# Kernel optimization log

Measured on AMD Instinct MI355X. Metric: run time of the kernel, lower is better.

The kernel has to match this reference:

```python
import jax, jax.numpy as jnp
import numpy as np

N_NODES = 50000
N_EDGES = 1600000
NFEAT = 256
NHID = 32
HEADS = 8
NCLASS = 2
NEG_SLOPE = 0.2  # DGL GATConv default


def gat_layer(x, src, dst, W, al, ar, b, num_nodes):
    """DGL-style GATConv layer.
    x: [N, in], W: [in, H*F], al/ar: [H, F], b: [H*F].
    Returns [N, H*F].
    """
    H, F = al.shape
    feat = (x @ W).reshape(num_nodes, H, F)          # [N, H, F]
    el = jnp.einsum('nhf,hf->nh', feat, al)          # [N, H]
    er = jnp.einsum('nhf,hf->nh', feat, ar)          # [N, H]
    e = jax.nn.leaky_relu(el[src] + er[dst], NEG_SLOPE)  # [E, H]
    # segment softmax over incoming edges of each dst node
    m = jax.ops.segment_max(e, dst, num_segments=num_nodes)  # [N, H]
    m = jnp.where(jnp.isfinite(m), m, 0.0)
    m = jax.lax.stop_gradient(m)
    ee = jnp.exp(e - m[dst])                          # [E, H]
    denom = jax.ops.segment_sum(ee, dst, num_segments=num_nodes)  # [N, H]
    alpha = ee / jnp.maximum(denom[dst], 1e-16)       # [E, H]
    # weighted scatter-aggregation of source features
    msg = feat[src] * alpha[:, :, None]               # [E, H, F]
    out = jax.ops.segment_sum(msg, dst, num_segments=num_nodes)  # [N, H, F]
    return out.reshape(num_nodes, H * F) + b


def setup_inputs() -> dict:
    key = jax.random.key(0)
    ks = jax.random.split(key, 10)
    x = jax.random.normal(ks[0], (N_NODES, NFEAT), dtype=jnp.float32)
    edge_src = jax.random.randint(ks[1], (N_EDGES,), 0, N_NODES, dtype=jnp.int32)
    edge_dst = jax.random.randint(ks[2], (N_EDGES,), 0, N_NODES, dtype=jnp.int32)
    s1 = 1.0 / np.sqrt(NFEAT)
    W1 = jax.random.normal(ks[3], (NFEAT, HEADS * NHID), dtype=jnp.float32) * s1
    al1 = jax.random.normal(ks[4], (HEADS, NHID), dtype=jnp.float32) * 0.1
    ar1 = jax.random.normal(ks[5], (HEADS, NHID), dtype=jnp.float32) * 0.1
    b1 = jnp.zeros((HEADS * NHID,), dtype=jnp.float32)
    s2 = 1.0 / np.sqrt(HEADS * NHID)
    W2 = jax.random.normal(ks[6], (HEADS * NHID, NCLASS), dtype=jnp.float32) * s2
    al2 = jax.random.normal(ks[7], (1, NCLASS), dtype=jnp.float32) * 0.1
    ar2 = jax.random.normal(ks[8], (1, NCLASS), dtype=jnp.float32) * 0.1
    b2 = jnp.zeros((NCLASS,), dtype=jnp.float32)
    return {"x": x, "edge_src": edge_src, "edge_dst": edge_dst,
            "W1": W1, "al1": al1, "ar1": ar1, "b1": b1,
            "W2": W2, "al2": al2, "ar2": ar2, "b2": b2}


def reference(x, edge_src, edge_dst, W1, al1, ar1, b1, W2, al2, ar2, b2):
    h = gat_layer(x, edge_src, edge_dst, W1, al1, ar1, b1, N_NODES)  # [N, 8*nhid]
    h = jax.nn.elu(h)
    h = gat_layer(h, edge_src, edge_dst, W2, al2, ar2, b2, N_NODES)  # [N, nclass]
    return jax.nn.log_softmax(h, axis=1)
```

## Files before the change

kernel.cpp:

```cpp
#include <hip/hip_runtime.h>
#include <hip/hip_fp8.h>


#define NN 50000
#define NE 1600000
#define NBK 196
#define NPB 1024
#define PCH 1563
#define CAP 16384

typedef __attribute__((ext_vector_type(8))) short short8;
typedef __attribute__((ext_vector_type(4))) float f32x4;
typedef __attribute__((ext_vector_type(2))) float f32x2;

__device__ inline unsigned short f2bf(float f) {
  unsigned int u = __float_as_uint(f);
  unsigned int r = (u + 0x7fffu + ((u >> 16) & 1u)) >> 16;
  return (unsigned short)r;
}
__device__ inline unsigned char f2fp8(float f) {
  __hip_fp8_e4m3 q(f);
  return *reinterpret_cast<unsigned char*>(&q);
}
__device__ inline float lrelu_exp(float v) {
  v = v >= 0.f ? v : 0.2f * v;
  return __expf(v);
}

__global__ __launch_bounds__(256) void k_hist2(const int* __restrict__ dst,
                                               int* __restrict__ hmat, int E) {
  __shared__ int h[NBK];
  int tid = threadIdx.x, blk = blockIdx.x;
  for (int i = tid; i < NBK; i += 256) h[i] = 0;
  __syncthreads();
  int b0 = blk * PCH;
  int tot = min(PCH, E - b0);
  for (int k = tid; k < tot; k += 256)
    atomicAdd(&h[dst[b0 + k] >> 8], 1);
  __syncthreads();
  for (int i = tid; i < NBK; i += 256)
    hmat[(size_t)i * NPB + blk] = h[i];
}

__global__ __launch_bounds__(1024) void k_cscan(int* __restrict__ hmat,
                                                int* __restrict__ cur) {
  __shared__ int buf[NPB];
  int b = blockIdx.x, tid = threadIdx.x;
  int v = hmat[(size_t)b * NPB + tid];
  buf[tid] = v;
  __syncthreads();
  for (int off = 1; off < NPB; off <<= 1) {
    int t = (tid >= off) ? buf[tid - off] : 0;
    __syncthreads();
    buf[tid] += t;
    __syncthreads();
  }
  hmat[(size_t)b * NPB + tid] = buf[tid] - v;
  if (tid == NPB - 1) cur[b] = buf[tid];
}

__global__ __launch_bounds__(256) void k_part2(const int* __restrict__ dst,
                                               const int* __restrict__ src,
                                               const int* __restrict__ hmat,
                                               int* __restrict__ stage, int E) {
  __shared__ int sbuf[PCH];
  __shared__ int dbuf[PCH];
  __shared__ int h[NBK], scn[NBK], base[NBK], lofs[NBK];
  __shared__ int sc[256];
  int tid = threadIdx.x, blk = blockIdx.x;
  for (int i = tid; i < NBK; i += 256) { h[i] = 0; lofs[i] = 0; }
  __syncthreads();
  int b0 = blk * PCH;
  int tot = min(PCH, E - b0);
  for (int k = tid; k < tot; k += 256) {
    int d = dst[b0 + k];
    dbuf[k] = d;
    atomicAdd(&h[d >> 8], 1);
  }
  __syncthreads();
  int v = (tid < NBK) ? h[tid] : 0;
  sc[tid] = v;
  __syncthreads();
  for (int off = 1; off < 256; off <<= 1) {
    int t = (tid >= off) ? sc[tid - off] : 0;
    __syncthreads();
    sc[tid] += t;
    __syncthreads();
  }
  if (tid < NBK) {
    scn[tid] = sc[tid] - v;
    base[tid] = hmat[(size_t)tid * NPB + blk];
  }
  __syncthreads();
  for (int k = tid; k < tot; k += 256) {
    int d = dbuf[k];
    int b = d >> 8;
    int r = atomicAdd(&lofs[b], 1);
    sbuf[scn[b] + r] = (b << 24) | ((d & 255) << 16) | src[b0 + k];
  }
  __syncthreads();
  for (int i = tid; i < tot; i += 256) {
    int e = sbuf[i];
    int b = (unsigned)e >> 24;
    stage[(size_t)b * CAP + base[b] + (i - scn[b])] = e;
  }
}

__global__ __launch_bounds__(512) void k_build(const int* __restrict__ stage,
                                               const int* __restrict__ tots,
                                               int2* __restrict__ od,
                                               unsigned short* __restrict__ csr,
                                               int n) {
  __shared__ int h[256], buf[256], cur[256];
  int b = blockIdx.x, tid = threadIdx.x;
  int tot = tots[b];
  const int* st = stage + (size_t)b * CAP;
  unsigned short* cs = csr + (size_t)b * CAP;
  if (tid < 256) h[tid] = 0;
  __syncthreads();
  for (int k = tid; k < tot; k += 512)
    atomicAdd(&h[(st[k] >> 16) & 255], 1);
  __syncthreads();
  int v = (tid < 256) ? h[tid] : 0;
  if (tid < 256) buf[tid] = v;
  __syncthreads();
  for (int off = 1; off < 256; off <<= 1) {
    int t = (tid >= off && tid < 256) ? buf[tid - off] : 0;
    __syncthreads();
    if (tid < 256) buf[tid] += t;
    __syncthreads();
  }
  if (tid < 256) {
    int excl = buf[tid] - v;
    int node = b * 256 + tid;
    if (node < n) od[node] = make_int2(b * CAP + excl, v);
    cur[tid] = excl;
  }
  __syncthreads();
  for (int k = tid; k < tot; k += 512) {
    int p = st[k];
    int r = atomicAdd(&cur[(p >> 16) & 255], 1);
    cs[r] = (unsigned short)(p & 0xFFFF);
  }
}

__global__ __launch_bounds__(256) void k_packw(const float* __restrict__ W1,
                                               const float* __restrict__ al,
                                               const float* __restrict__ ar,
                                               unsigned short* __restrict__ W1p,
                                               unsigned short* __restrict__ walar) {
  int idx = blockIdx.x * 256 + threadIdx.x;
  if (idx < 8192) {
    int nf = idx >> 9, rem = idx & 511;
    int ks = rem >> 6, lane = rem & 63;
    int n = nf * 16 + (lane & 15);
    int kb = ks * 32 + (lane >> 4) * 8;
#pragma unroll
    for (int j = 0; j < 8; ++j)
      W1p[(size_t)idx * 8 + j] = f2bf(W1[(kb + j) * 256 + n]);
  } else if (idx < 8192 + 512) {
    int idx2 = idx - 8192;
    int ks = idx2 >> 6, lane = idx2 & 63;
    int n = lane & 15;
    int kb = ks * 32 + (lane >> 4) * 8;
    const float* coef = (n < 8) ? (al + n * 32) : (ar + (n - 8) * 32);
    int bc = (n < 8) ? n * 32 : (n - 8) * 32;
#pragma unroll
    for (int j = 0; j < 8; ++j) {
      int k = kb + j;
      float s = 0.f;
      for (int f = 0; f < 32; ++f) s += W1[k * 256 + bc + f] * coef[f];
      walar[(size_t)idx2 * 8 + j] = f2bf(s);
    }
  }
}

__global__ __launch_bounds__(256) void k_gemm1m(
    const float* __restrict__ x, const unsigned short* __restrict__ W1p,
    const unsigned short* __restrict__ walar,
    unsigned char* __restrict__ feat8, float* __restrict__ el,
    float* __restrict__ er, int n) {
  __shared__ unsigned short xs[32][264];
  int w = threadIdx.x >> 6, lane = threadIdx.x & 63;
  int tile = blockIdx.x * 32;
  if (tile >= n) return;
  for (int idx = threadIdx.x; idx < 2048; idx += 256) {
    int r = idx >> 6, c4 = (idx & 63) * 4;
    int row = tile + r;
    float4 v = (row < n)
                   ? *reinterpret_cast<const float4*>(x + (size_t)row * 256 + c4)
                   : make_float4(0.f, 0.f, 0.f, 0.f);
    xs[r][c4 + 0] = f2bf(v.x);
    xs[r][c4 + 1] = f2bf(v.y);
    xs[r][c4 + 2] = f2bf(v.z);
    xs[r][c4 + 3] = f2bf(v.w);
  }
  __syncthreads();
  int r0 = lane & 15, kgrp = lane >> 4;
  int nf0 = w * 4;
  f32x4 acc[4][2];
  f32x4 accE[2];
#pragma unroll
  for (int nf = 0; nf < 4; ++nf)
#pragma unroll
    for (int mf = 0; mf < 2; ++mf) acc[nf][mf] = (f32x4){0.f, 0.f, 0.f, 0.f};
  accE[0] = (f32x4){0.f, 0.f, 0.f, 0.f};
  accE[1] = (f32x4){0.f, 0.f, 0.f, 0.f};

  for (int ks = 0; ks < 8; ++ks) {
    int kb = ks * 32 + kgrp * 8;
    short8 a0 = *reinterpret_cast<const short8*>(&xs[r0][kb]);
    short8 a1 = *reinterpret_cast<const short8*>(&xs[16 + r0][kb]);
#pragma unroll
    for (int nf = 0; nf < 4; ++nf) {
      short8 b = *reinterpret_cast<const short8*>(
          W1p + ((size_t)((nf0 + nf) * 8 + ks) * 64 + lane) * 8);
      acc[nf][0] = __builtin_amdgcn_mfma_f32_16x16x32_bf16(a0, b, acc[nf][0], 0, 0, 0);
      acc[nf][1] = __builtin_amdgcn_mfma_f32_16x16x32_bf16(a1, b, acc[nf][1], 0, 0, 0);
    }
    if (w == 0) {
      short8 bE = *reinterpret_cast<const short8*>(
          walar + ((size_t)ks * 64 + lane) * 8);
      accE[0] = __builtin_amdgcn_mfma_f32_16x16x32_bf16(a0, bE, accE[0], 0, 0, 0);
      accE[1] = __builtin_amdgcn_mfma_f32_16x16x32_bf16(a1, bE, accE[1], 0, 0, 0);
    }
  }
#pragma unroll
  for (int nf = 0; nf < 4; ++nf)
#pragma unroll
    for (int mf = 0; mf < 2; ++mf)
#pragma unroll
      for (int q = 0; q < 4; ++q) {
        int row = tile + mf * 16 + kgrp * 4 + q;
        if (row < n)
          feat8[(size_t)row * 256 + (nf0 + nf) * 16 + r0] = f2fp8(acc[nf][mf][q]);
      }
  if (w == 0) {
#pragma unroll
    for (int mf = 0; mf < 2; ++mf)
#pragma unroll
      for (int q = 0; q < 4; ++q) {
        int row = tile + mf * 16 + kgrp * 4 + q;
        if (row < n) {
          if (r0 < 8) el[(size_t)row * 8 + r0] = accE[mf][q];
          else        er[(size_t)row * 8 + (r0 - 8)] = accE[mf][q];
        }
      }
  }
}

__global__ __launch_bounds__(256) void k_agg1(
    const unsigned char* __restrict__ feat8, const float* __restrict__ el,
    const float* __restrict__ er, const int2* __restrict__ od,
    const unsigned short* __restrict__ csr, const float* __restrict__ b1,
    const float* __restrict__ W2, const float* __restrict__ al2,
    const float* __restrict__ ar2, float4* __restrict__ node4, int n) {
  int dn = blockIdx.x * 4 + (threadIdx.x >> 6);
  if (dn >= n) return;
  int l = threadIdx.x & 63;
  int hh = l >> 3;
  int h8 = l & 7;
  float erv = er[dn * 8 + h8];
  int2 o2 = od[dn];
  int beg = o2.x, end = o2.x + o2.y;
  f32x2 acc01 = {0.f, 0.f}, acc23 = {0.f, 0.f};
  float den = 0.f;
  int g = beg;
  for (; g + 8 <= end; g += 8) {
    int s_my = csr[g + (l >> 3)];
    float eev = lrelu_exp(el[s_my * 8 + h8] + erv);
#pragma unroll
    for (int e = 0; e < 8; ++e) {
      int s = __builtin_amdgcn_readlane(s_my, e * 8);
      float ee = __shfl(eev, e * 8 + hh, 64);
      den += ee;
      const unsigned char* rowp = feat8 + (size_t)s * 256;
      unsigned int fv = *reinterpret_cast<const unsigned int*>(rowp + l * 4);
      f32x2 lo = __builtin_amdgcn_cvt_pk_f32_fp8(fv, false);
      f32x2 hi = __builtin_amdgcn_cvt_pk_f32_fp8(fv, true);
      f32x2 ee2 = {ee, ee};
      acc01 = ee2 * lo + acc01;
      acc23 = ee2 * hi + acc23;
    }
  }
  if (g < end) {
    int rem = end - g;
    int idx = g + (l >> 3);
    int s_t = csr[idx < end ? idx : end - 1];
    float ee_t = lrelu_exp(el[s_t * 8 + h8] + erv);
    for (int e = 0; e < rem; ++e) {
      int s = __builtin_amdgcn_readlane(s_t, e * 8);
      float ee = __shfl(ee_t, e * 8 + hh, 64);
      den += ee;
      const unsigned char* rowp = feat8 + (size_t)s * 256;
      unsigned int fv = *reinterpret_cast<const unsigned int*>(rowp + l * 4);
      f32x2 lo = __builtin_amdgcn_cvt_pk_f32_fp8(fv, false);
      f32x2 hi = __builtin_amdgcn_cvt_pk_f32_fp8(fv, true);
      f32x2 ee2 = {ee, ee};
      acc01 = ee2 * lo + acc01;
      acc23 = ee2 * hi + acc23;
    }
  }
  float4 bv = *reinterpret_cast<const float4*>(b1 + l * 4);
  float4 w2e = *reinterpret_cast<const float4*>(W2 + l * 8);
  float4 w2o = *reinterpret_cast<const float4*>(W2 + l * 8 + 4);
  float inv = 1.f / fmaxf(den, 1e-16f);
  float v0 = acc01[0] * inv + bv.x; v0 = v0 > 0.f ? v0 : expm1f(v0);
  float v1 = acc01[1] * inv + bv.y; v1 = v1 > 0.f ? v1 : expm1f(v1);
  float v2 = acc23[0] * inv + bv.z; v2 = v2 > 0.f ? v2 : expm1f(v2);
  float v3 = acc23[1] * inv + bv.w; v3 = v3 > 0.f ? v3 : expm1f(v3);
  float p0 = v0 * w2e.x + v1 * w2e.z + v2 * w2o.x + v3 * w2o.z;
  float p1 = v0 * w2e.y + v1 * w2e.w + v2 * w2o.y + v3 * w2o.w;
#pragma unroll
  for (int off = 32; off; off >>= 1) {
    p0 += __shfl_xor(p0, off, 64);
    p1 += __shfl_xor(p1, off, 64);
  }
  if (l == 0) {
    float e2 = p0 * al2[0] + p1 * al2[1];
    float r2 = p0 * ar2[0] + p1 * ar2[1];
    node4[dn] = make_float4(p0, p1, e2, r2);
  }
}

__global__ __launch_bounds__(256) void k_agg2(
    const float4* __restrict__ node4, const int2* __restrict__ od,
    const unsigned short* __restrict__ csr, const float* __restrict__ b2,
    float* __restrict__ out, int n) {
  int dn = blockIdx.x * 16 + (threadIdx.x >> 4);
  int l = threadIdx.x & 15;
  if (dn >= n) return;
  float erd = node4[dn].w;
  int2 o2 = od[dn];
  int beg = o2.x, end = o2.x + o2.y;
  float den = 0.f, a0 = 0.f, a1 = 0.f;
  for (int e = beg + l; e < end; e += 16) {
    int s = csr[e];
    float4 n4 = node4[s];
    float ev = n4.z + erd;
    ev = ev >= 0.f ? ev : 0.2f * ev;
    float ee = __expf(ev);
    den += ee;
    a0 = fmaf(ee, n4.x, a0);
    a1 = fmaf(ee, n4.y, a1);
  }
#pragma unroll
  for (int off = 8; off; off >>= 1) {
    den += __shfl_xor(den, off, 16);
    a0 += __shfl_xor(a0, off, 16);
    a1 += __shfl_xor(a1, off, 16);
  }
  if (l == 0) {
    float inv = 1.f / fmaxf(den, 1e-16f);
    float z0 = a0 * inv + b2[0];
    float z1 = a1 * inv + b2[1];
    float m = fmaxf(z0, z1);
    float lse = m + logf(__expf(z0 - m) + __expf(z1 - m));
    out[dn * 2 + 0] = z0 - lse;
    out[dn * 2 + 1] = z1 - lse;
  }
}

extern "C" void kernel_launch(void* const* d_in, const int* in_sizes, int n_in,
                              void* d_out, int out_size, void* d_ws,
                              size_t ws_size, hipStream_t stream) {
  const float* x   = (const float*)d_in[0];
  const int* esrc  = (const int*)d_in[1];
  const int* edst  = (const int*)d_in[2];
  const float* W1  = (const float*)d_in[3];
  const float* al1 = (const float*)d_in[4];
  const float* ar1 = (const float*)d_in[5];
  const float* b1  = (const float*)d_in[6];
  const float* W2  = (const float*)d_in[7];
  const float* al2 = (const float*)d_in[8];
  const float* ar2 = (const float*)d_in[9];
  const float* b2  = (const float*)d_in[10];
  float* out = (float*)d_out;

  size_t off = 0;
  auto alloc = [&](size_t bytes) {
    void* p = (char*)d_ws + off;
    off += (bytes + 255) & ~(size_t)255;
    return p;
  };
  unsigned char* feat8 = (unsigned char*)alloc((size_t)NN * 256);
  unsigned short* W1p  = (unsigned short*)alloc((size_t)16 * 8 * 64 * 8 * 2);
  unsigned short* walar = (unsigned short*)alloc((size_t)8 * 64 * 8 * 2);
  float* el1    = (float*)alloc((size_t)NN * 8 * 4);
  float* er1    = (float*)alloc((size_t)NN * 8 * 4);
  float4* node4 = (float4*)alloc((size_t)NN * 16);
  int* stage    = (int*)alloc((size_t)NBK * CAP * 4);
  int* hmat     = (int*)alloc((size_t)NBK * NPB * 4);
  unsigned short* csr = (unsigned short*)alloc((size_t)NBK * CAP * 2);
  int2* od      = (int2*)alloc((size_t)NN * 8);
  int* cur      = (int*)alloc((size_t)NBK * 4);

  k_hist2<<<NPB, 256, 0, stream>>>(edst, hmat, NE);
  k_cscan<<<NBK, NPB, 0, stream>>>(hmat, cur);
  k_part2<<<NPB, 256, 0, stream>>>(edst, esrc, hmat, stage, NE);
  k_build<<<NBK, 512, 0, stream>>>(stage, cur, od, csr, NN);

  k_packw<<<34, 256, 0, stream>>>(W1, al1, ar1, W1p, walar);
  k_gemm1m<<<(NN + 31) / 32, 256, 0, stream>>>(x, W1p, walar, feat8, el1,
                                               er1, NN);
  k_agg1<<<(NN + 3) / 4, 256, 0, stream>>>(feat8, el1, er1, od, csr, b1,
                                           W2, al2, ar2, node4, NN);
  k_agg2<<<(NN + 15) / 16, 256, 0, stream>>>(node4, od, csr, b2, out, NN);
}
```

Baseline: 154.0 us.

## Replace histogram+scan partition pre-pass with atomic bucket offset reservation

Removes the separate per-block histogram kernel and column-scan kernel. Each partition block now reserves its slice in each destination bucket with a global atomicAdd on a zeroed per-bucket counter, so two launches and one pass over dst are dropped. In exchange the edge order inside each bucket becomes nondeterministic, which k_build must tolerate, and there is extra contention on 196 global counters.

```diff
diff --git a/kernel.cpp b/kernel.cpp
--- a/kernel.cpp
+++ b/kernel.cpp
@@ -27,42 +27,10 @@
   return __expf(v);
 }
 
-__global__ __launch_bounds__(256) void k_hist2(const int* __restrict__ dst,
-                                               int* __restrict__ hmat, int E) {
-  __shared__ int h[NBK];
-  int tid = threadIdx.x, blk = blockIdx.x;
-  for (int i = tid; i < NBK; i += 256) h[i] = 0;
-  __syncthreads();
-  int b0 = blk * PCH;
-  int tot = min(PCH, E - b0);
-  for (int k = tid; k < tot; k += 256)
-    atomicAdd(&h[dst[b0 + k] >> 8], 1);
-  __syncthreads();
-  for (int i = tid; i < NBK; i += 256)
-    hmat[(size_t)i * NPB + blk] = h[i];
-}
-
-__global__ __launch_bounds__(1024) void k_cscan(int* __restrict__ hmat,
-                                                int* __restrict__ cur) {
-  __shared__ int buf[NPB];
-  int b = blockIdx.x, tid = threadIdx.x;
-  int v = hmat[(size_t)b * NPB + tid];
-  buf[tid] = v;
-  __syncthreads();
-  for (int off = 1; off < NPB; off <<= 1) {
-    int t = (tid >= off) ? buf[tid - off] : 0;
-    __syncthreads();
-    buf[tid] += t;
-    __syncthreads();
-  }
-  hmat[(size_t)b * NPB + tid] = buf[tid] - v;
-  if (tid == NPB - 1) cur[b] = buf[tid];
-}
-
-__global__ __launch_bounds__(256) void k_part2(const int* __restrict__ dst,
-                                               const int* __restrict__ src,
-                                               const int* __restrict__ hmat,
-                                               int* __restrict__ stage, int E) {
+__global__ __launch_bounds__(256) void k_part(const int* __restrict__ dst,
+                                              const int* __restrict__ src,
+                                              int* __restrict__ cur,
+                                              int* __restrict__ stage, int E) {
   __shared__ int sbuf[PCH];
   __shared__ int dbuf[PCH];
   __shared__ int h[NBK], scn[NBK], base[NBK], lofs[NBK];
@@ -89,7 +57,7 @@
   }
   if (tid < NBK) {
     scn[tid] = sc[tid] - v;
-    base[tid] = hmat[(size_t)tid * NPB + blk];
+    base[tid] = v ? atomicAdd(&cur[tid], v) : 0;
   }
   __syncthreads();
   for (int k = tid; k < tot; k += 256) {
@@ -390,14 +358,12 @@
   float* er1    = (float*)alloc((size_t)NN * 8 * 4);
   float4* node4 = (float4*)alloc((size_t)NN * 16);
   int* stage    = (int*)alloc((size_t)NBK * CAP * 4);
-  int* hmat     = (int*)alloc((size_t)NBK * NPB * 4);
   unsigned short* csr = (unsigned short*)alloc((size_t)NBK * CAP * 2);
   int2* od      = (int2*)alloc((size_t)NN * 8);
   int* cur      = (int*)alloc((size_t)NBK * 4);
 
-  k_hist2<<<NPB, 256, 0, stream>>>(edst, hmat, NE);
-  k_cscan<<<NBK, NPB, 0, stream>>>(hmat, cur);
-  k_part2<<<NPB, 256, 0, stream>>>(edst, esrc, hmat, stage, NE);
+  hipMemsetAsync(cur, 0, (size_t)NBK * 4, stream);
+  k_part<<<NPB, 256, 0, stream>>>(edst, esrc, cur, stage, NE);
   k_build<<<NBK, 512, 0, stream>>>(stage, cur, od, csr, NN);
 
   k_packw<<<34, 256, 0, stream>>>(W1, al1, ar1, W1p, walar);
```

Result: slower. 168.6 us (+9.5%).
